# Optimization experiments

Hardware: AMD Instinct MI355X
Metric: run time of the kernel (lower is better)

Reference implementation:

```python
import jax, jax.numpy as jnp
import numpy as np

B, T, L_CTX = 64, 150, 256
H = 512   # decoder_num_hidden
E = 512   # target_embedding_size
V = 1000  # target_vocab_size


def setup_inputs() -> dict:
    key = jax.random.key(0)
    ks = jax.random.split(key, 10)
    s = 0.05
    return {
        "cnn_feats": jax.random.normal(ks[0], (B, L_CTX, H), dtype=jnp.float32),
        "seq": jax.random.randint(ks[1], (B, T), 0, V, dtype=jnp.int32),
        "embed_table": jax.random.normal(ks[2], (V, E), dtype=jnp.float32) * s,
        "W_ih": jax.random.normal(ks[3], (4 * H, E), dtype=jnp.float32) * s,
        "b_ih": jnp.zeros((4 * H,), dtype=jnp.float32),
        "W_hh": jax.random.normal(ks[4], (4 * H, H), dtype=jnp.float32) * s,
        "b_hh": jnp.zeros((4 * H,), dtype=jnp.float32),
        "W_hm": jax.random.normal(ks[5], (H, H), dtype=jnp.float32) * s,
        "W_om": jax.random.normal(ks[6], (H, 2 * H), dtype=jnp.float32) * s,
        "W_logit": jax.random.normal(ks[7], (V, H), dtype=jnp.float32) * s,
        "b_logit": jnp.zeros((V,), dtype=jnp.float32),
    }


def reference(cnn_feats, seq, embed_table, W_ih, b_ih, W_hh, b_hh,
              W_hm, W_om, W_logit, b_logit):
    # Single-layer LSTMCell decoder with per-step attention (eval mode, dropout=0).
    def step(carry, it):
        h, c = carry                      # [B,H] each
        xt = jax.nn.relu(embed_table[it])  # [B,E]
        gates = xt @ W_ih.T + b_ih + h @ W_hh.T + b_hh  # [B,4H]
        i, f, g, o = jnp.split(gates, 4, axis=1)
        c2 = jax.nn.sigmoid(f) * c + jax.nn.sigmoid(i) * jnp.tanh(g)
        h2 = jax.nn.sigmoid(o) * jnp.tanh(c2)
        mapped = h2 @ W_hm.T              # [B,H]
        attn = jnp.einsum("blh,bh->bl", cnn_feats, mapped)
        w = jax.nn.softmax(attn, axis=1)
        ctx = jnp.einsum("bl,blh->bh", w, cnn_feats)
        out = jnp.concatenate([ctx, h2], axis=1) @ W_om.T  # [B,H]
        logp = jax.nn.log_softmax(out @ W_logit.T + b_logit, axis=1)
        return (h2, c2), logp

    bsz = cnn_feats.shape[0]
    h0 = jnp.zeros((bsz, W_hh.shape[1]), dtype=cnn_feats.dtype)
    c0 = jnp.zeros_like(h0)
    _, outs = jax.lax.scan(step, (h0, c0), seq.T)  # outs: [T,B,V]
    return outs.transpose(1, 0, 2)  # [B,T,V]
```

## Files before the change

### kernel.cpp

```cpp
#include <hip/hip_runtime.h>
#include <math.h>

#define B_  64
#define T_  150
#define L_  256
#define H_  512
#define E_  512
#define V_  1000
#define G4_ 2048
#define DB_ 16
#define HCB 32

typedef _Float16 f16;
typedef f16   f16x8 __attribute__((ext_vector_type(8)));
typedef f16   f16x4 __attribute__((ext_vector_type(4)));
typedef float f32x4 __attribute__((ext_vector_type(4)));
typedef unsigned long long ull;

__device__ __forceinline__ float sigmf(float x) { return 1.0f / (1.0f + expf(-x)); }

__global__ __launch_bounds__(512) void decoder_mfma(
    const int*   __restrict__ seq,
    const float* __restrict__ G,
    const float* __restrict__ Whh,
    ull*  __restrict__ xh,
    int*  __restrict__ tags,
    float* __restrict__ hbuf)
{
    __shared__ f16   hlds[64][520];
    __shared__ float glds[64][132];
    __shared__ float csh[64][36];

    const int tid = threadIdx.x;
    const int bb  = blockIdx.x;
    const int ln  = tid & 63;
    const int wv  = tid >> 6;
    const int mh  = wv >> 2;
    const int nt2 = wv & 3;

    f16x8 bfr[2][16];
    #pragma unroll
    for (int j = 0; j < 2; ++j) {
        const int n = 2 * nt2 + j;
        const int grow = (n >> 1) * H_ + bb * HCB + (n & 1) * 16 + (ln & 15);
        #pragma unroll
        for (int kt = 0; kt < 16; ++kt) {
            const int k0 = kt * 32 + (ln >> 4) * 8;
            float4 w0 = *(const float4*)(Whh + (size_t)grow * H_ + k0);
            float4 w1 = *(const float4*)(Whh + (size_t)grow * H_ + k0 + 4);
            bfr[j][kt] = (f16x8){(f16)w0.x, (f16)w0.y, (f16)w0.z, (f16)w0.w,
                                 (f16)w1.x, (f16)w1.y, (f16)w1.z, (f16)w1.w};
        }
    }
    for (int e = tid; e < 64 * 520 / 4; e += 512) ((ull*)hlds)[e] = 0ull;
    for (int e = tid; e < 64 * 36; e += 512) ((float*)csh)[e] = 0.f;
    __syncthreads();

    const int cb = tid >> 3, cg = tid & 7;

    for (int t = 0; t < T_; ++t) {
        const int v = seq[cb * T_ + t];
        const float* gp = G + (size_t)v * G4_ + bb * HCB + cg * 4;
        float4 gq0 = *(const float4*)(gp);
        float4 gq1 = *(const float4*)(gp + H_);
        float4 gq2 = *(const float4*)(gp + 2 * H_);
        float4 gq3 = *(const float4*)(gp + 3 * H_);

        if (t > 0) {
            if (tid < DB_) {
                while (__hip_atomic_load(&tags[tid], __ATOMIC_RELAXED,
                                         __HIP_MEMORY_SCOPE_AGENT) < t) {}
            }
            __syncthreads();
            const ull* src = xh + (size_t)(t & 1) * 64 * 128;
            ull v0[8], v1[8];
            #pragma unroll
            for (int it = 0; it < 8; ++it) {
                const int e = tid + it * 512;
                const int b = e >> 6, s = e & 63;
                v0[it] = __hip_atomic_load(&src[b * 128 + 2 * s], __ATOMIC_RELAXED,
                                           __HIP_MEMORY_SCOPE_AGENT);
                v1[it] = __hip_atomic_load(&src[b * 128 + 2 * s + 1], __ATOMIC_RELAXED,
                                           __HIP_MEMORY_SCOPE_AGENT);
            }
            #pragma unroll
            for (int it = 0; it < 8; ++it) {
                const int e = tid + it * 512;
                const int b = e >> 6, s = e & 63;
                ull* dst = (ull*)&hlds[b][s * 8];
                dst[0] = v0[it]; dst[1] = v1[it];
            }
            __syncthreads();
        }

        f32x4 acc00 = {0.f,0.f,0.f,0.f}, acc01 = {0.f,0.f,0.f,0.f};
        f32x4 acc10 = {0.f,0.f,0.f,0.f}, acc11 = {0.f,0.f,0.f,0.f};
        #pragma unroll
        for (int kt = 0; kt < 16; ++kt) {
            const int ko = kt * 32 + (ln >> 4) * 8;
            f16x8 a0 = *(const f16x8*)&hlds[(2 * mh)     * 16 + (ln & 15)][ko];
            f16x8 a1 = *(const f16x8*)&hlds[(2 * mh + 1) * 16 + (ln & 15)][ko];
            acc00 = __builtin_amdgcn_mfma_f32_16x16x32_f16(a0, bfr[0][kt], acc00, 0, 0, 0);
            acc01 = __builtin_amdgcn_mfma_f32_16x16x32_f16(a0, bfr[1][kt], acc01, 0, 0, 0);
            acc10 = __builtin_amdgcn_mfma_f32_16x16x32_f16(a1, bfr[0][kt], acc10, 0, 0, 0);
            acc11 = __builtin_amdgcn_mfma_f32_16x16x32_f16(a1, bfr[1][kt], acc11, 0, 0, 0);
        }
        {
            const int r0 = (2 * mh) * 16 + (ln >> 4) * 4;
            const int r1 = (2 * mh + 1) * 16 + (ln >> 4) * 4;
            const int c0 = (2 * nt2) * 16 + (ln & 15);
            const int c1 = (2 * nt2 + 1) * 16 + (ln & 15);
            #pragma unroll
            for (int i = 0; i < 4; ++i) {
                glds[r0 + i][c0] = acc00[i];
                glds[r0 + i][c1] = acc01[i];
                glds[r1 + i][c0] = acc10[i];
                glds[r1 + i][c1] = acc11[i];
            }
        }
        __syncthreads();

        {
            float4 Gi = *(const float4*)&glds[cb][cg * 4];
            float4 Gf = *(const float4*)&glds[cb][32 + cg * 4];
            float4 Gg = *(const float4*)&glds[cb][64 + cg * 4];
            float4 Go = *(const float4*)&glds[cb][96 + cg * 4];
            float4 cold = *(const float4*)&csh[cb][cg * 4];
            float gi[4] = {Gi.x + gq0.x, Gi.y + gq0.y, Gi.z + gq0.z, Gi.w + gq0.w};
            float gf[4] = {Gf.x + gq1.x, Gf.y + gq1.y, Gf.z + gq1.z, Gf.w + gq1.w};
            float gg[4] = {Gg.x + gq2.x, Gg.y + gq2.y, Gg.z + gq2.z, Gg.w + gq2.w};
            float go[4] = {Go.x + gq3.x, Go.y + gq3.y, Go.z + gq3.z, Go.w + gq3.w};
            float cl[4] = {cold.x, cold.y, cold.z, cold.w};
            float4 cnew, hnew;
            f16x4 hp;
            #pragma unroll
            for (int i = 0; i < 4; ++i) {
                float c2 = sigmf(gf[i]) * cl[i] + sigmf(gi[i]) * tanhf(gg[i]);
                float h2 = sigmf(go[i]) * tanhf(c2);
                ((float*)&cnew)[i] = c2;
                ((float*)&hnew)[i] = h2;
                hp[i] = (f16)h2;
            }
            *(float4*)&csh[cb][cg * 4] = cnew;
            *(float4*)&hbuf[((size_t)t * 64 + cb) * H_ + bb * HCB + cg * 4] = hnew;
            __hip_atomic_store(
                &xh[(size_t)((t + 1) & 1) * 64 * 128 + cb * 128 + bb * 8 + cg],
                __builtin_bit_cast(ull, hp),
                __ATOMIC_RELAXED, __HIP_MEMORY_SCOPE_AGENT);
        }
        __syncthreads();
        if (tid == 0)
            __hip_atomic_store(&tags[bb], t + 1, __ATOMIC_RELAXED,
                               __HIP_MEMORY_SCOPE_AGENT);
    }
}

template<bool RELU_A, bool REMAP>
__global__ __launch_bounds__(256) void gemm16_nt(
    const float* __restrict__ A1, const float* __restrict__ A2,
    const float* __restrict__ Bm,
    const float* __restrict__ bias1, const float* __restrict__ bias2,
    float* __restrict__ C, int M, int N, int KA)
{
    __shared__ f16 As[64][40];
    __shared__ f16 Bs[64][40];
    const int tid = threadIdx.x;
    const int m0 = blockIdx.x * 64, n0 = blockIdx.y * 64;
    const int ln = tid & 63, wv = tid >> 6;
    const int lr = tid >> 2, lc8 = (tid & 3) * 8;
    const int K = A2 ? 2 * KA : KA;
    f32x4 acc[4] = {};

    for (int kb = 0; kb < K; kb += 32) {
        const float* Ap; int kk;
        if (kb < KA) { Ap = A1; kk = kb; } else { Ap = A2; kk = kb - KA; }
        int gm = m0 + lr;
        float4 a0 = make_float4(0.f, 0.f, 0.f, 0.f), a1 = a0;
        if (gm < M) {
            a0 = *(const float4*)(Ap + (size_t)gm * KA + kk + lc8);
            a1 = *(const float4*)(Ap + (size_t)gm * KA + kk + lc8 + 4);
        }
        if (RELU_A) {
            a0.x = fmaxf(a0.x, 0.f); a0.y = fmaxf(a0.y, 0.f);
            a0.z = fmaxf(a0.z, 0.f); a0.w = fmaxf(a0.w, 0.f);
            a1.x = fmaxf(a1.x, 0.f); a1.y = fmaxf(a1.y, 0.f);
            a1.z = fmaxf(a1.z, 0.f); a1.w = fmaxf(a1.w, 0.f);
        }
        f16x8 av = {(f16)a0.x, (f16)a0.y, (f16)a0.z, (f16)a0.w,
                    (f16)a1.x, (f16)a1.y, (f16)a1.z, (f16)a1.w};
        *(f16x8*)&As[lr][lc8] = av;

        int gn = n0 + lr;
        float4 b0 = make_float4(0.f, 0.f, 0.f, 0.f), b1 = b0;
        if (gn < N) {
            b0 = *(const float4*)(Bm + (size_t)gn * K + kb + lc8);
            b1 = *(const float4*)(Bm + (size_t)gn * K + kb + lc8 + 4);
        }
        f16x8 bv = {(f16)b0.x, (f16)b0.y, (f16)b0.z, (f16)b0.w,
                    (f16)b1.x, (f16)b1.y, (f16)b1.z, (f16)b1.w};
        *(f16x8*)&Bs[lr][lc8] = bv;
        __syncthreads();

        f16x8 af = *(const f16x8*)&As[wv * 16 + (ln & 15)][(ln >> 4) * 8];
        #pragma unroll
        for (int ntt = 0; ntt < 4; ++ntt) {
            f16x8 bf = *(const f16x8*)&Bs[ntt * 16 + (ln & 15)][(ln >> 4) * 8];
            acc[ntt] = __builtin_amdgcn_mfma_f32_16x16x32_f16(af, bf, acc[ntt], 0, 0, 0);
        }
        __syncthreads();
    }

    #pragma unroll
    for (int ntt = 0; ntt < 4; ++ntt)
        #pragma unroll
        for (int i = 0; i < 4; ++i) {
            int gm = m0 + wv * 16 + (ln >> 4) * 4 + i;
            int gn = n0 + ntt * 16 + (ln & 15);
            if (gm < M && gn < N) {
                float v = acc[ntt][i];
                if (bias1) v += bias1[gn];
                if (bias2) v += bias2[gn];
                size_t row = REMAP ? ((size_t)(gm & 63) * T_ + (gm >> 6)) : (size_t)gm;
                C[row * (size_t)N + gn] = v;
            }
        }
}

__global__ __launch_bounds__(512) void score_softmax(
    const float* __restrict__ mapped,
    const float* __restrict__ cnn,
    f16* __restrict__ attP)
{
    __shared__ f16   As[64][40];
    __shared__ f16   Bs[256][40];
    __shared__ float sl[64][260];

    const int tid = threadIdx.x;
    const int m0  = blockIdx.x * 64;
    const int b   = blockIdx.y;
    const int ln  = tid & 63, wv = tid >> 6;
    const int mh  = wv >> 2, nq = wv & 3;
    const int ln15 = ln & 15, ln4 = (ln >> 4) * 8;
    const float* cnnb = cnn + (size_t)b * L_ * H_;

    f32x4 acc[2][4] = {};

    for (int kb = 0; kb < H_; kb += 32) {
        {
            int lr = tid >> 3, lc4 = (tid & 7) * 4;
            int t = m0 + lr;
            float4 a = make_float4(0.f, 0.f, 0.f, 0.f);
            if (t < T_) a = *(const float4*)(mapped + ((size_t)t * 64 + b) * H_ + kb + lc4);
            As[lr][lc4 + 0] = (f16)a.x; As[lr][lc4 + 1] = (f16)a.y;
            As[lr][lc4 + 2] = (f16)a.z; As[lr][lc4 + 3] = (f16)a.w;
        }
        {
            int br = tid >> 1, bc16 = (tid & 1) * 16;
            const float* src = cnnb + (size_t)br * H_ + kb + bc16;
            float4 w0 = *(const float4*)(src);
            float4 w1 = *(const float4*)(src + 4);
            float4 w2 = *(const float4*)(src + 8);
            float4 w3 = *(const float4*)(src + 12);
            f16x8 p0 = {(f16)w0.x, (f16)w0.y, (f16)w0.z, (f16)w0.w,
                        (f16)w1.x, (f16)w1.y, (f16)w1.z, (f16)w1.w};
            f16x8 p1 = {(f16)w2.x, (f16)w2.y, (f16)w2.z, (f16)w2.w,
                        (f16)w3.x, (f16)w3.y, (f16)w3.z, (f16)w3.w};
            *(f16x8*)&Bs[br][bc16]     = p0;
            *(f16x8*)&Bs[br][bc16 + 8] = p1;
        }
        __syncthreads();

        f16x8 a0 = *(const f16x8*)&As[(2 * mh)     * 16 + ln15][ln4];
        f16x8 a1 = *(const f16x8*)&As[(2 * mh + 1) * 16 + ln15][ln4];
        #pragma unroll
        for (int nj = 0; nj < 4; ++nj) {
            f16x8 bf = *(const f16x8*)&Bs[(nq * 4 + nj) * 16 + ln15][ln4];
            acc[0][nj] = __builtin_amdgcn_mfma_f32_16x16x32_f16(a0, bf, acc[0][nj], 0, 0, 0);
            acc[1][nj] = __builtin_amdgcn_mfma_f32_16x16x32_f16(a1, bf, acc[1][nj], 0, 0, 0);
        }
        __syncthreads();
    }

    #pragma unroll
    for (int mi = 0; mi < 2; ++mi)
        #pragma unroll
        for (int nj = 0; nj < 4; ++nj)
            #pragma unroll
            for (int i = 0; i < 4; ++i)
                sl[(2 * mh + mi) * 16 + (ln >> 4) * 4 + i][(nq * 4 + nj) * 16 + ln15]
                    = acc[mi][nj][i];
    __syncthreads();

    #pragma unroll
    for (int rr = 0; rr < 8; ++rr) {
        int r = wv * 8 + rr;
        int t = m0 + r;
        if (t < T_) {
            float4 v = *(const float4*)&sl[r][ln * 4];
            float mx = fmaxf(fmaxf(v.x, v.y), fmaxf(v.z, v.w));
            #pragma unroll
            for (int off = 32; off; off >>= 1) mx = fmaxf(mx, __shfl_xor(mx, off));
            float e0 = expf(v.x - mx), e1 = expf(v.y - mx);
            float e2 = expf(v.z - mx), e3 = expf(v.w - mx);
            float s = e0 + e1 + e2 + e3;
            #pragma unroll
            for (int off = 32; off; off >>= 1) s += __shfl_xor(s, off);
            float inv = 1.f / s;
            f16x4 p = {(f16)(e0 * inv), (f16)(e1 * inv), (f16)(e2 * inv), (f16)(e3 * inv)};
            *(f16x4*)(attP + ((size_t)b * T_ + t) * L_ + ln * 4) = p;
        }
    }
}

__global__ __launch_bounds__(256) void ctx16_nn(
    const f16* __restrict__ attP,
    const float* __restrict__ cnn,
    float* __restrict__ ctxout)
{
    __shared__ f16 As[64][40];
    __shared__ f16 Bs[64][40];
    const int tid = threadIdx.x;
    const int m0 = blockIdx.x * 64, n0 = blockIdx.y * 64;
    const int b  = blockIdx.z;
    const int ln = tid & 63, wv = tid >> 6;
    const int ln15 = ln & 15, ln4 = (ln >> 4) * 8;
    const float* cnnb = cnn + (size_t)b * L_ * H_;
    const f16*   pb   = attP + (size_t)b * T_ * L_;
    f32x4 acc[4] = {};

    for (int kb = 0; kb < L_; kb += 32) {
        {
            int lr = tid >> 2, lc8 = (tid & 3) * 8;
            int t = m0 + lr;
            f16x8 av = {};
            if (t < T_) av = *(const f16x8*)(pb + (size_t)t * L_ + kb + lc8);
            *(f16x8*)&As[lr][lc8] = av;
        }
        {
            int br = tid >> 3;
            int nc = (tid & 7) * 8;
            const float* src = cnnb + (size_t)(kb + br) * H_ + n0 + nc;
            float4 w0 = *(const float4*)(src);
            float4 w1 = *(const float4*)(src + 4);
            float wv8[8] = {w0.x, w0.y, w0.z, w0.w, w1.x, w1.y, w1.z, w1.w};
            #pragma unroll
            for (int j = 0; j < 8; ++j) Bs[nc + j][br] = (f16)wv8[j];
        }
        __syncthreads();

        f16x8 af = *(const f16x8*)&As[wv * 16 + ln15][ln4];
        #pragma unroll
        for (int ntt = 0; ntt < 4; ++ntt) {
            f16x8 bf = *(const f16x8*)&Bs[ntt * 16 + ln15][ln4];
            acc[ntt] = __builtin_amdgcn_mfma_f32_16x16x32_f16(af, bf, acc[ntt], 0, 0, 0);
        }
        __syncthreads();
    }

    #pragma unroll
    for (int ntt = 0; ntt < 4; ++ntt)
        #pragma unroll
        for (int i = 0; i < 4; ++i) {
            int t  = m0 + wv * 16 + (ln >> 4) * 4 + i;
            int gn = n0 + ntt * 16 + ln15;
            if (t < T_)
                ctxout[(size_t)b * H_ + (size_t)t * (B_ * H_) + gn] = acc[ntt][i];
        }
}

__global__ __launch_bounds__(256) void logsoftmax_k(float* __restrict__ out)
{
    const int row = blockIdx.x;
    float* p = out + (size_t)row * V_;
    const int tid = threadIdx.x, lane = tid & 63, wave = tid >> 6;
    __shared__ float red[8];

    float vals[4];
    int n = 0;
    float mx = -INFINITY;
    for (int v = tid; v < V_; v += 256) { vals[n] = p[v]; mx = fmaxf(mx, vals[n]); ++n; }
    #pragma unroll
    for (int off = 32; off; off >>= 1) mx = fmaxf(mx, __shfl_xor(mx, off));
    if (lane == 0) red[wave] = mx;
    __syncthreads();
    mx = fmaxf(fmaxf(red[0], red[1]), fmaxf(red[2], red[3]));

    float s = 0.f;
    for (int i = 0; i < n; ++i) s += expf(vals[i] - mx);
    #pragma unroll
    for (int off = 32; off; off >>= 1) s += __shfl_xor(s, off);
    if (lane == 0) red[4 + wave] = s;
    __syncthreads();
    s = red[4] + red[5] + red[6] + red[7];

    const float lse = mx + logf(s);
    n = 0;
    for (int v = tid; v < V_; v += 256) { p[v] = vals[n] - lse; ++n; }
}

extern "C" void kernel_launch(void* const* d_in, const int* in_sizes, int n_in,
                              void* d_out, int out_size, void* d_ws, size_t ws_size,
                              hipStream_t stream)
{
    const float* cnn     = (const float*)d_in[0];
    const int*   seq     = (const int*)d_in[1];
    const float* embed   = (const float*)d_in[2];
    const float* W_ih    = (const float*)d_in[3];
    const float* b_ih    = (const float*)d_in[4];
    const float* W_hh    = (const float*)d_in[5];
    const float* b_hh    = (const float*)d_in[6];
    const float* W_hm    = (const float*)d_in[7];
    const float* W_om    = (const float*)d_in[8];
    const float* W_logit = (const float*)d_in[9];
    const float* b_logit = (const float*)d_in[10];
    float* out = (float*)d_out;

    float* ws = (float*)d_ws;
    float* G    = ws;
    float* hbuf = G + (size_t)V_ * G4_;
    float* outv = hbuf + (size_t)B_ * T_ * H_;
    ull*   xh   = (ull*)(outv + (size_t)B_ * T_ * H_);
    int*   tags = (int*)(xh + 2 * 64 * 128);
    float* mapped = out;
    f16*   attP   = (f16*)(out + (size_t)B_ * T_ * H_);

    hipMemsetAsync(tags, 0, DB_ * sizeof(int), stream);

    gemm16_nt<true, false><<<dim3(16, 32), 256, 0, stream>>>(
        embed, nullptr, W_ih, b_ih, b_hh, G, V_, G4_, E_);

    decoder_mfma<<<DB_, 512, 0, stream>>>(seq, G, W_hh, xh, tags, hbuf);

    gemm16_nt<false, false><<<dim3(150, 8), 256, 0, stream>>>(
        hbuf, nullptr, W_hm, nullptr, nullptr, mapped, B_ * T_, H_, H_);
    score_softmax<<<dim3(3, 64), 512, 0, stream>>>(mapped, cnn, attP);
    ctx16_nn<<<dim3(3, 8, 64), 256, 0, stream>>>(attP, cnn, mapped);
    gemm16_nt<false, false><<<dim3(150, 8), 256, 0, stream>>>(
        mapped, hbuf, W_om, nullptr, nullptr, outv, B_ * T_, H_, H_);
    gemm16_nt<false, true><<<dim3(150, 16), 256, 0, stream>>>(
        outv, nullptr, W_logit, b_logit, nullptr, out, B_ * T_, V_, H_);
    logsoftmax_k<<<B_ * T_, 256, 0, stream>>>(out);
}
```

Before: 1.021 ms.

## Halve recurrent decoder block count by doubling hidden columns per block

The persistent LSTM recurrence kernel now uses 8 blocks instead of 16, each owning 64 hidden units (256 gate columns). Each wave computes all 64 batch rows against two column tiles, and each thread handles 8 hidden units. The aim is to cut the cost of the per-step cross-block flag spin and barrier synchronization, which dominates a latency-bound recurrence. In exchange each block does twice the MFMA and elementwise work per step, and fewer CUs are used.

Measured after the change: 1.421 ms. 39.2% more time.

```diff
diff --git a/kernel.cpp b/kernel.cpp
--- a/kernel.cpp
+++ b/kernel.cpp
@@ -8,8 +8,8 @@
 #define E_  512
 #define V_  1000
 #define G4_ 2048
-#define DB_ 16
-#define HCB 32
+#define DB_ 8
+#define HCB 64
 
 typedef _Float16 f16;
 typedef f16   f16x8 __attribute__((ext_vector_type(8)));
@@ -28,24 +28,25 @@
     float* __restrict__ hbuf)
 {
     __shared__ f16   hlds[64][520];
-    __shared__ float glds[64][132];
-    __shared__ float csh[64][36];
+    __shared__ float glds[64][260];
+    __shared__ float csh[64][68];
 
     const int tid = threadIdx.x;
     const int bb  = blockIdx.x;
     const int ln  = tid & 63;
     const int wv  = tid >> 6;
-    const int mh  = wv >> 2;
-    const int nt2 = wv & 3;
+    const int ln15 = ln & 15;
+    const int lnk8 = (ln >> 4) * 8;
+    const int lr4  = (ln >> 4) * 4;
 
     f16x8 bfr[2][16];
     #pragma unroll
     for (int j = 0; j < 2; ++j) {
-        const int n = 2 * nt2 + j;
-        const int grow = (n >> 1) * H_ + bb * HCB + (n & 1) * 16 + (ln & 15);
+        const int n = 2 * wv + j;
+        const int grow = (n >> 2) * H_ + bb * HCB + (n & 3) * 16 + ln15;
         #pragma unroll
         for (int kt = 0; kt < 16; ++kt) {
-            const int k0 = kt * 32 + (ln >> 4) * 8;
+            const int k0 = kt * 32 + lnk8;
             float4 w0 = *(const float4*)(Whh + (size_t)grow * H_ + k0);
             float4 w1 = *(const float4*)(Whh + (size_t)grow * H_ + k0 + 4);
             bfr[j][kt] = (f16x8){(f16)w0.x, (f16)w0.y, (f16)w0.z, (f16)w0.w,
@@ -53,18 +54,20 @@
         }
     }
     for (int e = tid; e < 64 * 520 / 4; e += 512) ((ull*)hlds)[e] = 0ull;
-    for (int e = tid; e < 64 * 36; e += 512) ((float*)csh)[e] = 0.f;
+    for (int e = tid; e < 64 * 68; e += 512) ((float*)csh)[e] = 0.f;
     __syncthreads();
 
     const int cb = tid >> 3, cg = tid & 7;
 
     for (int t = 0; t < T_; ++t) {
         const int v = seq[cb * T_ + t];
-        const float* gp = G + (size_t)v * G4_ + bb * HCB + cg * 4;
-        float4 gq0 = *(const float4*)(gp);
-        float4 gq1 = *(const float4*)(gp + H_);
-        float4 gq2 = *(const float4*)(gp + 2 * H_);
-        float4 gq3 = *(const float4*)(gp + 3 * H_);
+        const float* gp = G + (size_t)v * G4_ + bb * HCB + cg * 8;
+        float4 ga[4][2];
+        #pragma unroll
+        for (int q = 0; q < 4; ++q) {
+            ga[q][0] = *(const float4*)(gp + q * H_);
+            ga[q][1] = *(const float4*)(gp + q * H_ + 4);
+        }
 
         if (t > 0) {
             if (tid < DB_) {
@@ -93,60 +96,67 @@
             __syncthreads();
         }
 
-        f32x4 acc00 = {0.f,0.f,0.f,0.f}, acc01 = {0.f,0.f,0.f,0.f};
-        f32x4 acc10 = {0.f,0.f,0.f,0.f}, acc11 = {0.f,0.f,0.f,0.f};
+        f32x4 acc[4][2] = {};
         #pragma unroll
         for (int kt = 0; kt < 16; ++kt) {
-            const int ko = kt * 32 + (ln >> 4) * 8;
-            f16x8 a0 = *(const f16x8*)&hlds[(2 * mh)     * 16 + (ln & 15)][ko];
-            f16x8 a1 = *(const f16x8*)&hlds[(2 * mh + 1) * 16 + (ln & 15)][ko];
-            acc00 = __builtin_amdgcn_mfma_f32_16x16x32_f16(a0, bfr[0][kt], acc00, 0, 0, 0);
-            acc01 = __builtin_amdgcn_mfma_f32_16x16x32_f16(a0, bfr[1][kt], acc01, 0, 0, 0);
-            acc10 = __builtin_amdgcn_mfma_f32_16x16x32_f16(a1, bfr[0][kt], acc10, 0, 0, 0);
-            acc11 = __builtin_amdgcn_mfma_f32_16x16x32_f16(a1, bfr[1][kt], acc11, 0, 0, 0);
-        }
+            const int ko = kt * 32 + lnk8;
+            f16x8 a0 = *(const f16x8*)&hlds[0 * 16 + ln15][ko];
+            f16x8 a1 = *(const f16x8*)&hlds[1 * 16 + ln15][ko];
+            f16x8 a2 = *(const f16x8*)&hlds[2 * 16 + ln15][ko];
+            f16x8 a3 = *(const f16x8*)&hlds[3 * 16 + ln15][ko];
+            #pragma unroll
+            for (int j = 0; j < 2; ++j) {
+                acc[0][j] = __builtin_amdgcn_mfma_f32_16x16x32_f16(a0, bfr[j][kt], acc[0][j], 0, 0, 0);
+                acc[1][j] = __builtin_amdgcn_mfma_f32_16x16x32_f16(a1, bfr[j][kt], acc[1][j], 0, 0, 0);
+                acc[2][j] = __builtin_amdgcn_mfma_f32_16x16x32_f16(a2, bfr[j][kt], acc[2][j], 0, 0, 0);
+                acc[3][j] = __builtin_amdgcn_mfma_f32_16x16x32_f16(a3, bfr[j][kt], acc[3][j], 0, 0, 0);
+            }
+        }
+        #pragma unroll
+        for (int m = 0; m < 4; ++m)
+            #pragma unroll
+            for (int j = 0; j < 2; ++j)
+                #pragma unroll
+                for (int i = 0; i < 4; ++i)
+                    glds[m * 16 + lr4 + i][(2 * wv + j) * 16 + ln15] = acc[m][j][i];
+        __syncthreads();
+
         {
-            const int r0 = (2 * mh) * 16 + (ln >> 4) * 4;
-            const int r1 = (2 * mh + 1) * 16 + (ln >> 4) * 4;
-            const int c0 = (2 * nt2) * 16 + (ln & 15);
-            const int c1 = (2 * nt2 + 1) * 16 + (ln & 15);
-            #pragma unroll
-            for (int i = 0; i < 4; ++i) {
-                glds[r0 + i][c0] = acc00[i];
-                glds[r0 + i][c1] = acc01[i];
-                glds[r1 + i][c0] = acc10[i];
-                glds[r1 + i][c1] = acc11[i];
-            }
-        }
-        __syncthreads();
-
-        {
-            float4 Gi = *(const float4*)&glds[cb][cg * 4];
-            float4 Gf = *(const float4*)&glds[cb][32 + cg * 4];
-            float4 Gg = *(const float4*)&glds[cb][64 + cg * 4];
-            float4 Go = *(const float4*)&glds[cb][96 + cg * 4];
-            float4 cold = *(const float4*)&csh[cb][cg * 4];
-            float gi[4] = {Gi.x + gq0.x, Gi.y + gq0.y, Gi.z + gq0.z, Gi.w + gq0.w};
-            float gf[4] = {Gf.x + gq1.x, Gf.y + gq1.y, Gf.z + gq1.z, Gf.w + gq1.w};
-            float gg[4] = {Gg.x + gq2.x, Gg.y + gq2.y, Gg.z + gq2.z, Gg.w + gq2.w};
-            float go[4] = {Go.x + gq3.x, Go.y + gq3.y, Go.z + gq3.z, Go.w + gq3.w};
-            float cl[4] = {cold.x, cold.y, cold.z, cold.w};
-            float4 cnew, hnew;
-            f16x4 hp;
-            #pragma unroll
-            for (int i = 0; i < 4; ++i) {
+            float gi[8], gf[8], gg[8], go[8], cl[8];
+            #pragma unroll
+            for (int hh = 0; hh < 2; ++hh) {
+                float4 Gi = *(const float4*)&glds[cb][0 * 64 + cg * 8 + hh * 4];
+                float4 Gf = *(const float4*)&glds[cb][1 * 64 + cg * 8 + hh * 4];
+                float4 Gg = *(const float4*)&glds[cb][2 * 64 + cg * 8 + hh * 4];
+                float4 Go = *(const float4*)&glds[cb][3 * 64 + cg * 8 + hh * 4];
+                float4 cc = *(const float4*)&csh[cb][cg * 8 + hh * 4];
+                #pragma unroll
+                for (int i = 0; i < 4; ++i) {
+                    gi[hh * 4 + i] = ((const float*)&Gi)[i] + ((const float*)&ga[0][hh])[i];
+                    gf[hh * 4 + i] = ((const float*)&Gf)[i] + ((const float*)&ga[1][hh])[i];
+                    gg[hh * 4 + i] = ((const float*)&Gg)[i] + ((const float*)&ga[2][hh])[i];
+                    go[hh * 4 + i] = ((const float*)&Go)[i] + ((const float*)&ga[3][hh])[i];
+                    cl[hh * 4 + i] = ((const float*)&cc)[i];
+                }
+            }
+            float hv[8], cv[8];
+            f16x8 hp;
+            #pragma unroll
+            for (int i = 0; i < 8; ++i) {
                 float c2 = sigmf(gf[i]) * cl[i] + sigmf(gi[i]) * tanhf(gg[i]);
                 float h2 = sigmf(go[i]) * tanhf(c2);
-                ((float*)&cnew)[i] = c2;
-                ((float*)&hnew)[i] = h2;
-                hp[i] = (f16)h2;
-            }
-            *(float4*)&csh[cb][cg * 4] = cnew;
-            *(float4*)&hbuf[((size_t)t * 64 + cb) * H_ + bb * HCB + cg * 4] = hnew;
-            __hip_atomic_store(
-                &xh[(size_t)((t + 1) & 1) * 64 * 128 + cb * 128 + bb * 8 + cg],
-                __builtin_bit_cast(ull, hp),
-                __ATOMIC_RELAXED, __HIP_MEMORY_SCOPE_AGENT);
+                cv[i] = c2; hv[i] = h2; hp[i] = (f16)h2;
+            }
+            *(float4*)&csh[cb][cg * 8]     = make_float4(cv[0], cv[1], cv[2], cv[3]);
+            *(float4*)&csh[cb][cg * 8 + 4] = make_float4(cv[4], cv[5], cv[6], cv[7]);
+            float* hb = hbuf + ((size_t)t * 64 + cb) * H_ + bb * HCB + cg * 8;
+            *(float4*)hb       = make_float4(hv[0], hv[1], hv[2], hv[3]);
+            *(float4*)(hb + 4) = make_float4(hv[4], hv[5], hv[6], hv[7]);
+            ull* dst = &xh[(size_t)((t + 1) & 1) * 64 * 128 + cb * 128 + bb * 16 + cg * 2];
+            __hip_atomic_store(&dst[0], ((const ull*)&hp)[0],
+                               __ATOMIC_RELAXED, __HIP_MEMORY_SCOPE_AGENT);
+            __hip_atomic_store(&dst[1], ((const ull*)&hp)[1],
+                               __ATOMIC_RELAXED, __HIP_MEMORY_SCOPE_AGENT);
         }
         __syncthreads();
         if (tid == 0)
```
